# Kernel optimization log

Measured on AMD Instinct MI355X. Metric: run time of the kernel, lower is better.

## Reference

```python
import jax, jax.numpy as jnp
import numpy as np

DIM = 2048
N_HEADS = 16
Q_LORA = 1536
KV_LORA = 512
NOPE = 128
ROPE = 64
QK_D = NOPE + ROPE  # 192
V_D = 128
EPS = 1e-6
B, S = 2, 2048


def rmsnorm(x, w, eps=EPS):
    return x * jax.lax.rsqrt(jnp.mean(x * x, axis=-1, keepdims=True) + eps) * w


def rotate_pe(x, cos, sin):
    # x: [B, S, H, ROPE]; cos/sin: [S, ROPE] -> broadcast [1, S, 1, ROPE]
    c = cos[None, :, None, :]
    s = sin[None, :, None, :]
    x1, x2 = jnp.split(x, 2, axis=-1)
    rot = jnp.concatenate([-x2, x1], axis=-1)
    return x * c + rot * s


def setup_inputs() -> dict:
    key = jax.random.key(0)
    ks = jax.random.split(key, 8)
    std = 0.02
    x = jax.random.normal(ks[0], (B, S, DIM), dtype=jnp.float32)
    # proper rotary tables
    inv_freq = 1.0 / (10000.0 ** (np.arange(0, ROPE, 2, dtype=np.float32) / ROPE))
    t = np.arange(S, dtype=np.float32)
    freqs = np.outer(t, inv_freq)  # [S, ROPE/2]
    emb = np.concatenate([freqs, freqs], axis=-1)  # [S, ROPE]
    cos = jnp.asarray(np.cos(emb))
    sin = jnp.asarray(np.sin(emb))
    wq_a = jax.random.normal(ks[1], (Q_LORA, DIM), dtype=jnp.float32) * std
    q_norm_w = jnp.ones((Q_LORA,), dtype=jnp.float32)
    wq_b = jax.random.normal(ks[2], (N_HEADS * QK_D, Q_LORA), dtype=jnp.float32) * std
    wkv_a = jax.random.normal(ks[3], (KV_LORA + ROPE, DIM), dtype=jnp.float32) * std
    kv_norm_w = jnp.ones((KV_LORA,), dtype=jnp.float32)
    wkv_b = jax.random.normal(ks[4], (N_HEADS * (NOPE + V_D), KV_LORA), dtype=jnp.float32) * std
    wo = jax.random.normal(ks[5], (DIM, N_HEADS * V_D), dtype=jnp.float32) * std
    return {"x": x, "cos": cos, "sin": sin, "wq_a": wq_a, "q_norm_w": q_norm_w,
            "wq_b": wq_b, "wkv_a": wkv_a, "kv_norm_w": kv_norm_w, "wkv_b": wkv_b, "wo": wo}


def mla_forward(x, cos, sin, wq_a, q_norm_w, wq_b, wkv_a, kv_norm_w, wkv_b, wo):
    bsz, seqlen, _ = x.shape
    scale = QK_D ** (-0.5)
    # Q path: low-rank down-proj -> RMSNorm -> up-proj
    q = rmsnorm(x @ wq_a.T, q_norm_w) @ wq_b.T
    q = q.reshape(bsz, seqlen, N_HEADS, QK_D)
    q_nope, q_pe = q[..., :NOPE], q[..., NOPE:]
    q_pe = rotate_pe(q_pe, cos, sin)
    q = jnp.concatenate([q_nope, q_pe], axis=-1)
    # KV path: shared low-rank latent + single rope slice
    kv = x @ wkv_a.T  # [B, S, KV_LORA + ROPE]
    kv_c, k_pe = kv[..., :KV_LORA], kv[..., KV_LORA:]
    k_pe = rotate_pe(k_pe[:, :, None, :], cos, sin)  # [B, S, 1, ROPE]
    kvb = rmsnorm(kv_c, kv_norm_w) @ wkv_b.T
    kvb = kvb.reshape(bsz, seqlen, N_HEADS, NOPE + V_D)
    k_nope, v = kvb[..., :NOPE], kvb[..., NOPE:]
    k = jnp.concatenate([k_nope, jnp.broadcast_to(k_pe, (bsz, seqlen, N_HEADS, ROPE))], axis=-1)
    # causal attention
    scores = jnp.einsum('bqhd,bkhd->bhqk', q, k) * scale
    mask = jnp.tril(jnp.ones((seqlen, seqlen), dtype=bool))
    scores = jnp.where(mask[None, None], scores, jnp.finfo(scores.dtype).min)
    p = jax.nn.softmax(scores, axis=-1)
    out = jnp.einsum('bhqk,bkhd->bqhd', p, v)
    out = out.reshape(bsz, seqlen, N_HEADS * V_D)
    return out @ wo.T


def reference(x, cos, sin, wq_a, q_norm_w, wq_b, wkv_a, kv_norm_w, wkv_b, wo):
    return mla_forward(x, cos, sin, wq_a, q_norm_w, wq_b, wkv_a, kv_norm_w, wkv_b, wo)
```

## Files before the change

kernel.cpp:

```cpp
#include <hip/hip_runtime.h>

typedef unsigned short u16;
typedef __attribute__((ext_vector_type(8))) short short8;
typedef __attribute__((ext_vector_type(4))) float floatx4;

__device__ __forceinline__ float bf2f(u16 u) {
  union { unsigned int i; float f; } v; v.i = ((unsigned int)u) << 16; return v.f;
}
__device__ __forceinline__ u16 f2bf(float f) {
  union { float f; unsigned int i; } v; v.f = f;
  unsigned int u = v.i;
  u += 0x7fffu + ((u >> 16) & 1u);
  return (u16)(u >> 16);
}

__device__ __forceinline__ void gld_lds16(const void* g, void* l) {
  __builtin_amdgcn_global_load_lds(
      (const __attribute__((address_space(1))) unsigned int*)g,
      (__attribute__((address_space(3))) unsigned int*)l, 16, 0, 0);
}

__global__ __launch_bounds__(256) void repack_all_k(
    const float* __restrict__ x, const float* __restrict__ wqa,
    const float* __restrict__ wkva, const float* __restrict__ wqb,
    const float* __restrict__ wkvb, const float* __restrict__ wo,
    u16* __restrict__ xb, u16* __restrict__ wcat, u16* __restrict__ wqbb,
    u16* __restrict__ wkbb, u16* __restrict__ wob) {
  long i = ((long)blockIdx.x * 256 + threadIdx.x) * 4;
  int region = blockIdx.y;
  const float* s = nullptr; u16* d = nullptr; long n = 0;
  switch (region) {
    case 0: s = x;    d = xb;   n = 4096L * 2048; break;
    case 1: s = nullptr; d = wcat; n = 2176L * 2048; break;
    case 2: s = wqb;  d = wqbb; n = 3072L * 1536; break;
    case 3: s = wkvb; d = wkbb; n = 4096L * 512;  break;
    case 4: s = wo;   d = wob;  n = 2048L * 2048; break;
  }
  if (i >= n) return;
  float4 v;
  if (region == 1) {
    long r = i >> 11, c = i & 2047;
    if (r < 1536)      v = *(const float4*)(wqa + r * 2048 + c);
    else if (r < 2112) v = *(const float4*)(wkva + (r - 1536) * 2048 + c);
    else               v = (float4){0.f, 0.f, 0.f, 0.f};
  } else {
    v = *(const float4*)(s + i);
  }
  d[i + 0] = f2bf(v.x); d[i + 1] = f2bf(v.y);
  d[i + 2] = f2bf(v.z); d[i + 3] = f2bf(v.w);
}

template <int OUT_F32>
__device__ __forceinline__ void gemm_tile(
    const u16* __restrict__ A, int lda, const u16* __restrict__ W, int ldw,
    void* __restrict__ Cv, int ldc, int K, int bm, int bn,
    u16* Asm, u16* Bsm) {
  int tid = threadIdx.x;
  int lane = tid & 63, w = tid >> 6;
  int wm = (w >> 1) * 64, wn = (w & 1) * 64;

  floatx4 acc[4][4];
#pragma unroll
  for (int i = 0; i < 4; i++)
#pragma unroll
    for (int j = 0; j < 4; j++) acc[i][j] = (floatx4){0.f, 0.f, 0.f, 0.f};

  int sr = lane >> 2;
  int sc = (lane & 3) * 8;
  int fr = lane & 15;
  int fq = (lane >> 4) * 8;

  for (int k0 = 0; k0 < K; k0 += 32) {
#pragma unroll
    for (int c = 0; c < 2; c++) {
      int row = 32 * w + 16 * c + sr;
      gld_lds16(A + (size_t)(bm + row) * lda + k0 + sc, &Asm[(32 * w + 16 * c) * 32]);
      gld_lds16(W + (size_t)(bn + row) * ldw + k0 + sc, &Bsm[(32 * w + 16 * c) * 32]);
    }
    __syncthreads();
    short8 af[4], bfr[4];
#pragma unroll
    for (int i = 0; i < 4; i++)
      af[i] = *(const short8*)&Asm[(wm + i * 16 + fr) * 32 + fq];
#pragma unroll
    for (int j = 0; j < 4; j++)
      bfr[j] = *(const short8*)&Bsm[(wn + j * 16 + fr) * 32 + fq];
#pragma unroll
    for (int i = 0; i < 4; i++)
#pragma unroll
      for (int j = 0; j < 4; j++)
        acc[i][j] = __builtin_amdgcn_mfma_f32_16x16x32_bf16(af[i], bfr[j], acc[i][j], 0, 0, 0);
    __syncthreads();
  }

  int cr = (lane >> 4) * 4, cc = lane & 15;
#pragma unroll
  for (int i = 0; i < 4; i++)
#pragma unroll
    for (int j = 0; j < 4; j++) {
      int col = bn + wn + j * 16 + cc;
#pragma unroll
      for (int r = 0; r < 4; r++) {
        size_t row = (size_t)(bm + wm + i * 16 + cr + r);
        if (OUT_F32) ((float*)Cv)[row * ldc + col] = acc[i][j][r];
        else         ((u16*)Cv)[row * ldc + col] = f2bf(acc[i][j][r]);
      }
    }
}

template <int OUT_F32>
__global__ __launch_bounds__(256) void gemm_bt_mfma(
    const u16* __restrict__ A, int lda,
    const u16* __restrict__ W, int ldw,
    void* __restrict__ Cv, int ldc, int K) {
  __shared__ u16 Asm[128 * 32];
  __shared__ u16 Bsm[128 * 32];
  gemm_tile<OUT_F32>(A, lda, W, ldw, Cv, ldc, K, blockIdx.y * 128, blockIdx.x * 128, Asm, Bsm);
}

__global__ __launch_bounds__(256) void gemm_dual_mfma(
    const u16* __restrict__ A1, int lda1, const u16* __restrict__ W1, int ldw1,
    u16* __restrict__ C1, int ldc1, int K1, int nt1,
    const u16* __restrict__ A2, int lda2, const u16* __restrict__ W2, int ldw2,
    u16* __restrict__ C2, int ldc2, int K2) {
  __shared__ u16 Asm[128 * 32];
  __shared__ u16 Bsm[128 * 32];
  int bx = blockIdx.x;
  if (bx < nt1)
    gemm_tile<0>(A1, lda1, W1, ldw1, C1, ldc1, K1, blockIdx.y * 128, bx * 128, Asm, Bsm);
  else
    gemm_tile<0>(A2, lda2, W2, ldw2, C2, ldc2, K2, blockIdx.y * 128, (bx - nt1) * 128, Asm, Bsm);
}

__global__ __launch_bounds__(256) void normrope_k(
    u16* __restrict__ qkv, const float* __restrict__ qnw,
    const float* __restrict__ kvnw, const float* __restrict__ cosb,
    const float* __restrict__ sinb, int S) {
  int row = blockIdx.x, tid = threadIdx.x;
  u16* p = qkv + (size_t)row * 2176;
  float s1 = 0.f, s2 = 0.f;
#pragma unroll
  for (int it = 0; it < 6; it++) { float v = bf2f(p[tid + 256 * it]); s1 += v * v; }
#pragma unroll
  for (int it = 0; it < 2; it++) { float v = bf2f(p[1536 + tid + 256 * it]); s2 += v * v; }
  for (int off = 32; off > 0; off >>= 1) {
    s1 += __shfl_down(s1, off);
    s2 += __shfl_down(s2, off);
  }
  __shared__ float red1[4], red2[4];
  if ((tid & 63) == 0) { red1[tid >> 6] = s1; red2[tid >> 6] = s2; }
  __syncthreads();
  float inv1 = rsqrtf((red1[0] + red1[1] + red1[2] + red1[3]) / 1536.f + 1e-6f);
  float inv2 = rsqrtf((red2[0] + red2[1] + red2[2] + red2[3]) / 512.f + 1e-6f);
#pragma unroll
  for (int it = 0; it < 6; it++) {
    int i = tid + 256 * it;
    p[i] = f2bf(bf2f(p[i]) * inv1 * qnw[i]);
  }
#pragma unroll
  for (int it = 0; it < 2; it++) {
    int i = tid + 256 * it;
    p[1536 + i] = f2bf(bf2f(p[1536 + i]) * inv2 * kvnw[i]);
  }
  if (tid < 32) {
    int pos = row % S;
    float c1 = cosb[pos * 64 + tid];
    float c2 = cosb[pos * 64 + tid + 32];
    float sn1 = sinb[pos * 64 + tid];
    float sn2 = sinb[pos * 64 + tid + 32];
    float x1 = bf2f(p[2048 + tid]), x2 = bf2f(p[2048 + tid + 32]);
    p[2048 + tid]      = f2bf(x1 * c1 - x2 * sn1);
    p[2048 + tid + 32] = f2bf(x2 * c2 + x1 * sn2);
  }
}

__global__ __launch_bounds__(256) void rope_k(
    u16* __restrict__ base, int row_stride, int head_stride, int head_off,
    const float* __restrict__ cosb, const float* __restrict__ sinb, int S) {
  int t = blockIdx.x;
  int h = blockIdx.y * 8 + (threadIdx.x >> 5);
  int i = threadIdx.x & 31;
  int pos = t % S;
  u16* p = base + (size_t)t * row_stride + h * head_stride + head_off;
  float c1 = cosb[pos * 64 + i];
  float c2 = cosb[pos * 64 + i + 32];
  float s1 = sinb[pos * 64 + i];
  float s2 = sinb[pos * 64 + i + 32];
  float x1 = bf2f(p[i]), x2 = bf2f(p[i + 32]);
  p[i]      = f2bf(x1 * c1 - x2 * s1);
  p[i + 32] = f2bf(x2 * c2 + x1 * s2);
}

__global__ __launch_bounds__(256) void vtrans_k(
    const u16* __restrict__ kvb, u16* __restrict__ vt, int S) {
  int tb = blockIdx.x, h = blockIdx.y, b = blockIdx.z;
  __shared__ __align__(16) u16 Ts[64][136];
  int tid = threadIdx.x;
#pragma unroll
  for (int it = 0; it < 4; it++) {
    int e = tid + 256 * it;
    int tok = e >> 4, c = e & 15;
    short8 v = *(const short8*)(kvb + (size_t)(b * S + tb * 64 + tok) * 4096 + h * 256 + 128 + c * 8);
    *(short8*)&Ts[tok][c * 8] = v;
  }
  __syncthreads();
  int vd = tid >> 1, half = (tid & 1) * 32;
  u16 tmp[32];
#pragma unroll
  for (int j = 0; j < 32; j++) tmp[j] = Ts[half + j][vd];
  u16* dst = vt + ((size_t)((b * 16 + h) * 128) + vd) * S + tb * 64 + half;
#pragma unroll
  for (int c = 0; c < 4; c++)
    *(short8*)(dst + c * 8) = *(short8*)&tmp[c * 8];
}

#define AT_BK 64
__global__ __launch_bounds__(256) void attn_mfma(
    const u16* __restrict__ qf, const u16* __restrict__ kvb,
    const u16* __restrict__ kpe, int kpe_stride, const u16* __restrict__ vt,
    u16* __restrict__ at, int S) {
  int id = blockIdx.x;
  int pair = id >> 5, hb = id & 31;
  int h = hb & 15, b = hb >> 4;
  int NT = S / AT_BK;
  int tid = threadIdx.x, lane = tid & 63, w = tid >> 6;
  int fr = lane & 15, fq = lane >> 4;
  int fs = fr & 7;

  __shared__ __align__(16) u16 Ksn[AT_BK * 128];
  __shared__ __align__(16) u16 Ksp[AT_BK * 64];
  __shared__ __align__(16) u16 Vts[128 * AT_BK];
  __shared__ __align__(16) u16 Ps[64 * AT_BK];

  const float scale = 0.07216878364870323f;

  for (int p = 0; p < 2; p++) {
    int qt = p ? (NT - 1 - pair) : pair;
    int q0 = qt * 64;

    short8 qfrag[6];
    {
      const u16* qrow = qf + (size_t)(b * S + q0 + w * 16 + fr) * 3072 + h * 192 + fq * 8;
#pragma unroll
      for (int ks = 0; ks < 6; ks++) qfrag[ks] = *(const short8*)(qrow + ks * 32);
    }

    floatx4 acc_o[8];
#pragma unroll
    for (int j = 0; j < 8; j++) acc_o[j] = (floatx4){0.f, 0.f, 0.f, 0.f};
    float m_r[4], l_r[4];
#pragma unroll
    for (int r = 0; r < 4; r++) { m_r[r] = -3e38f; l_r[r] = 0.f; }

    for (int kt = 0; kt <= qt; kt++) {
      int k0 = kt * AT_BK;
      size_t tokbase = (size_t)(b * S + k0);
#pragma unroll
      for (int c = 0; c < 4; c++) {
        int row = w * 16 + c * 4 + (lane >> 4);
        int cg = (lane & 15) ^ (row & 7);
        gld_lds16(kvb + (tokbase + row) * 4096 + h * 256 + cg * 8,
                  &Ksn[(w * 16 + c * 4) * 128]);
      }
#pragma unroll
      for (int c = 0; c < 2; c++) {
        int row = w * 16 + c * 8 + (lane >> 3);
        int cg = (lane & 7) ^ (row & 7);
        gld_lds16(kpe + (tokbase + row) * kpe_stride + cg * 8,
                  &Ksp[(w * 16 + c * 8) * 64]);
      }
#pragma unroll
      for (int c = 0; c < 4; c++) {
        int vd = w * 32 + c * 8 + (lane >> 3);
        int cg = (lane & 7) ^ (vd & 7);
        gld_lds16(vt + ((size_t)((b * 16 + h) * 128) + vd) * S + k0 + cg * 8,
                  &Vts[(w * 32 + c * 8) * 64]);
      }
      __syncthreads();

      floatx4 accs[4];
#pragma unroll
      for (int nt = 0; nt < 4; nt++) accs[nt] = (floatx4){0.f, 0.f, 0.f, 0.f};
      __builtin_amdgcn_s_setprio(1);
#pragma unroll
      for (int nt = 0; nt < 4; nt++) {
#pragma unroll
        for (int ks = 0; ks < 4; ks++) {
          short8 bf = *(const short8*)&Ksn[(nt * 16 + fr) * 128 + ((ks * 4 + fq) ^ fs) * 8];
          accs[nt] = __builtin_amdgcn_mfma_f32_16x16x32_bf16(qfrag[ks], bf, accs[nt], 0, 0, 0);
        }
#pragma unroll
        for (int ks = 0; ks < 2; ks++) {
          short8 bf = *(const short8*)&Ksp[(nt * 16 + fr) * 64 + ((ks * 4 + fq) ^ fs) * 8];
          accs[nt] = __builtin_amdgcn_mfma_f32_16x16x32_bf16(qfrag[4 + ks], bf, accs[nt], 0, 0, 0);
        }
      }
      __builtin_amdgcn_s_setprio(0);

      bool diag = (kt == qt);
#pragma unroll
      for (int nt = 0; nt < 4; nt++)
#pragma unroll
        for (int r = 0; r < 4; r++) {
          float s = accs[nt][r] * scale;
          if (diag) {
            int col = nt * 16 + fr;
            int row = fq * 4 + r;
            if (k0 + col > q0 + w * 16 + row) s = -3e38f;
          }
          accs[nt][r] = s;
        }

      float mx4[4];
      int grow = 0;
#pragma unroll
      for (int r = 0; r < 4; r++) {
        float mx = fmaxf(fmaxf(accs[0][r], accs[1][r]), fmaxf(accs[2][r], accs[3][r]));
        mx = fmaxf(mx, __shfl_xor(mx, 1));
        mx = fmaxf(mx, __shfl_xor(mx, 2));
        mx = fmaxf(mx, __shfl_xor(mx, 4));
        mx = fmaxf(mx, __shfl_xor(mx, 8));
        mx4[r] = mx;
        grow |= (mx > m_r[r] + 8.f) ? 1 : 0;
      }
      bool resc = __any(grow);
      float alpha[4];
      if (resc) {
#pragma unroll
        for (int r = 0; r < 4; r++) {
          float mnew = fmaxf(m_r[r], mx4[r]);
          alpha[r] = __expf(m_r[r] - mnew);
          m_r[r] = mnew;
          l_r[r] *= alpha[r];
        }
      }
#pragma unroll
      for (int nt = 0; nt < 4; nt++)
#pragma unroll
        for (int r = 0; r < 4; r++) {
          float pv = __expf(accs[nt][r] - m_r[r]);
          l_r[r] += pv;
          int row_p = w * 16 + fq * 4 + r;
          int col = nt * 16 + fr;
          Ps[row_p * 64 + (((col >> 3) ^ (row_p & 7)) * 8) + (col & 7)] = f2bf(pv);
        }
      __syncthreads();

      if (resc) {
#pragma unroll
        for (int j = 0; j < 8; j++)
#pragma unroll
          for (int r = 0; r < 4; r++) acc_o[j][r] *= alpha[r];
      }
      short8 pf0 = *(const short8*)&Ps[(w * 16 + fr) * 64 + (fq ^ fs) * 8];
      short8 pf1 = *(const short8*)&Ps[(w * 16 + fr) * 64 + ((4 + fq) ^ fs) * 8];
      __builtin_amdgcn_s_setprio(1);
#pragma unroll
      for (int j = 0; j < 8; j++) {
        short8 v0 = *(const short8*)&Vts[(j * 16 + fr) * 64 + (fq ^ fs) * 8];
        short8 v1 = *(const short8*)&Vts[(j * 16 + fr) * 64 + ((4 + fq) ^ fs) * 8];
        acc_o[j] = __builtin_amdgcn_mfma_f32_16x16x32_bf16(pf0, v0, acc_o[j], 0, 0, 0);
        acc_o[j] = __builtin_amdgcn_mfma_f32_16x16x32_bf16(pf1, v1, acc_o[j], 0, 0, 0);
      }
      __builtin_amdgcn_s_setprio(0);
      __syncthreads();
    }

    float inv_l[4];
#pragma unroll
    for (int r = 0; r < 4; r++) {
      float sm = l_r[r];
      sm += __shfl_xor(sm, 1);
      sm += __shfl_xor(sm, 2);
      sm += __shfl_xor(sm, 4);
      sm += __shfl_xor(sm, 8);
      inv_l[r] = 1.f / sm;
    }
#pragma unroll
    for (int j = 0; j < 8; j++)
#pragma unroll
      for (int r = 0; r < 4; r++) {
        size_t row = (size_t)(b * S + q0 + w * 16 + fq * 4 + r);
        at[row * 2048 + h * 128 + j * 16 + fr] = f2bf(acc_o[j][r] * inv_l[r]);
      }
  }
}

extern "C" void kernel_launch(void* const* d_in, const int* in_sizes, int n_in,
                              void* d_out, int out_size, void* d_ws, size_t ws_size,
                              hipStream_t stream) {
  (void)in_sizes; (void)n_in; (void)out_size; (void)ws_size;
  const float* x     = (const float*)d_in[0];
  const float* cosb  = (const float*)d_in[1];
  const float* sinb  = (const float*)d_in[2];
  const float* wq_a  = (const float*)d_in[3];
  const float* qnw   = (const float*)d_in[4];
  const float* wq_b  = (const float*)d_in[5];
  const float* wkv_a = (const float*)d_in[6];
  const float* kvnw  = (const float*)d_in[7];
  const float* wkv_b = (const float*)d_in[8];
  const float* wo    = (const float*)d_in[9];
  float* out = (float*)d_out;
  const int B = 2, S = 2048, T = B * S;

  char* wsb = (char*)d_ws;
  size_t off = 0;
  u16* xb   = (u16*)(wsb + off); off += (size_t)T * 2048 * 2;
  u16* wcat = (u16*)(wsb + off); off += (size_t)2176 * 2048 * 2;
  u16* wqbb = (u16*)(wsb + off); off += (size_t)3072 * 1536 * 2;
  u16* wkbb = (u16*)(wsb + off); off += (size_t)4096 * 512 * 2;
  u16* wob  = (u16*)(wsb + off); off += (size_t)2048 * 2048 * 2;
  u16* qkv  = (u16*)(wsb + off); off += (size_t)T * 2176 * 2;
  u16* qf   = (u16*)(wsb + off); off += (size_t)T * 3072 * 2;
  u16* kvb  = (u16*)(wsb + off); off += (size_t)T * 4096 * 2;
  u16* at   = (u16*)(wsb + off); off += (size_t)T * 2048 * 2;
  u16* vt   = xb;

  repack_all_k<<<dim3(8192, 5), 256, 0, stream>>>(
      x, wq_a, wkv_a, wq_b, wkv_b, wo, xb, wcat, wqbb, wkbb, wob);

  gemm_bt_mfma<0><<<dim3(2176 / 128, T / 128), 256, 0, stream>>>(xb, 2048, wcat, 2048, qkv, 2176, 2048);
  normrope_k<<<T, 256, 0, stream>>>(qkv, qnw, kvnw, cosb, sinb, S);
  gemm_dual_mfma<<<dim3(3072 / 128 + 4096 / 128, T / 128), 256, 0, stream>>>(
      qkv, 2176, wqbb, 1536, qf, 3072, 1536, 3072 / 128,
      qkv + 1536, 2176, wkbb, 512, kvb, 4096, 512);
  rope_k<<<dim3(T, 2), 256, 0, stream>>>(qf, 3072, 192, 128, cosb, sinb, S);
  vtrans_k<<<dim3(S / 64, 16, B), 256, 0, stream>>>(kvb, vt, S);
  attn_mfma<<<dim3((S / 128) * 32), 256, 0, stream>>>(qf, kvb, qkv + 2048, 2176, vt, at, S);
  gemm_bt_mfma<1><<<dim3(2048 / 128, T / 128), 256, 0, stream>>>(at, 2048, wob, 2048, out, 2048, 2048);
}
```

Measured before the change: 468.3 us.

## Replace GEMMs with 256x256 double-buffered swizzled-LDS pipelined MFMA kernel

All dense projections now use a 256x256 tile kernel with 512 threads, 64-wide K slabs held in double-buffered LDS with an XOR swizzle. Global-to-LDS loads for the next slab are issued between MFMA phases, with explicit waitcnt, barriers and setprio. The q/kv latent buffer is padded from 2176 to 2304 columns so the first GEMM tiles evenly. This aims to raise data reuse per load, avoid LDS bank conflicts, and overlap memory traffic with compute. The cost is more LDS per block (128 KB), fewer blocks in the grid, and some wasted compute on the zero-padded columns.

```diff
diff --git a/kernel.cpp b/kernel.cpp
--- a/kernel.cpp
+++ b/kernel.cpp
@@ -31,7 +31,7 @@
   const float* s = nullptr; u16* d = nullptr; long n = 0;
   switch (region) {
     case 0: s = x;    d = xb;   n = 4096L * 2048; break;
-    case 1: s = nullptr; d = wcat; n = 2176L * 2048; break;
+    case 1: s = nullptr; d = wcat; n = 2304L * 2048; break;
     case 2: s = wqb;  d = wqbb; n = 3072L * 1536; break;
     case 3: s = wkvb; d = wkbb; n = 4096L * 512;  break;
     case 4: s = wo;   d = wob;  n = 2048L * 2048; break;
@@ -50,86 +50,155 @@
   d[i + 2] = f2bf(v.z); d[i + 3] = f2bf(v.w);
 }
 
+#define SBAR()   __builtin_amdgcn_s_barrier()
+#define SCHED0() __builtin_amdgcn_sched_barrier(0)
+
+#define GPHASE(LAc, LBc, QQ, STAGE_STMT, WAIT_STMT)                              \
+  {                                                                              \
+    short8 a00 = *(const short8*)&(LAc)[agbase + (2*(QQ)) * 1024 + g0];          \
+    short8 a01 = *(const short8*)&(LAc)[agbase + (2*(QQ)) * 1024 + g1];          \
+    short8 a10 = *(const short8*)&(LAc)[agbase + (2*(QQ)+1) * 1024 + g0];        \
+    short8 a11 = *(const short8*)&(LAc)[agbase + (2*(QQ)+1) * 1024 + g1];        \
+    if ((QQ) == 0) {                                                             \
+      _Pragma("unroll")                                                          \
+      for (int fj = 0; fj < 4; ++fj) {                                           \
+        bfrg[fj][0] = *(const short8*)&(LBc)[bgbase + fj * 1024 + g0];           \
+        bfrg[fj][1] = *(const short8*)&(LBc)[bgbase + fj * 1024 + g1];           \
+      }                                                                          \
+    }                                                                            \
+    STAGE_STMT;                                                                  \
+    WAIT_STMT;                                                                   \
+    SCHED0();                                                                    \
+    SBAR();                                                                      \
+    asm volatile("s_waitcnt lgkmcnt(0)" ::: "memory");                           \
+    SCHED0();                                                                    \
+    __builtin_amdgcn_s_setprio(1);                                               \
+    _Pragma("unroll")                                                            \
+    for (int fj = 0; fj < 4; ++fj) {                                             \
+      acc[2*(QQ)][fj]   = __builtin_amdgcn_mfma_f32_16x16x32_bf16(a00, bfrg[fj][0], acc[2*(QQ)][fj],   0, 0, 0); \
+      acc[2*(QQ)][fj]   = __builtin_amdgcn_mfma_f32_16x16x32_bf16(a01, bfrg[fj][1], acc[2*(QQ)][fj],   0, 0, 0); \
+      acc[2*(QQ)+1][fj] = __builtin_amdgcn_mfma_f32_16x16x32_bf16(a10, bfrg[fj][0], acc[2*(QQ)+1][fj], 0, 0, 0); \
+      acc[2*(QQ)+1][fj] = __builtin_amdgcn_mfma_f32_16x16x32_bf16(a11, bfrg[fj][1], acc[2*(QQ)+1][fj], 0, 0, 0); \
+    }                                                                            \
+    __builtin_amdgcn_s_setprio(0);                                               \
+    SCHED0();                                                                    \
+    SBAR();                                                                      \
+  }
+
 template <int OUT_F32>
-__device__ __forceinline__ void gemm_tile(
+__device__ __forceinline__ void gemm256_tile(
     const u16* __restrict__ A, int lda, const u16* __restrict__ W, int ldw,
     void* __restrict__ Cv, int ldc, int K, int bm, int bn,
-    u16* Asm, u16* Bsm) {
+    u16* __restrict__ LA, u16* __restrict__ LB) {
   int tid = threadIdx.x;
   int lane = tid & 63, w = tid >> 6;
-  int wm = (w >> 1) * 64, wn = (w & 1) * 64;
-
-  floatx4 acc[4][4];
-#pragma unroll
-  for (int i = 0; i < 4; i++)
+  int wr = w >> 2, wc = w & 3;
+  int fr = lane & 15, fq = lane >> 4;
+
+  int srow = lane >> 3;
+  int sgl  = (lane & 7) ^ srow;
+
+  int agbase = (wr * 128 + fr) * 64;
+  int bgbase = (wc * 64 + fr) * 64;
+  int g0 = ((0 * 4 + fq) ^ (fr & 7)) * 8;
+  int g1 = ((1 * 4 + fq) ^ (fr & 7)) * 8;
+
+  floatx4 acc[8][4];
+#pragma unroll
+  for (int i = 0; i < 8; i++)
 #pragma unroll
     for (int j = 0; j < 4; j++) acc[i][j] = (floatx4){0.f, 0.f, 0.f, 0.f};
 
-  int sr = lane >> 2;
-  int sc = (lane & 3) * 8;
-  int fr = lane & 15;
-  int fq = (lane >> 4) * 8;
-
-  for (int k0 = 0; k0 < K; k0 += 32) {
-#pragma unroll
-    for (int c = 0; c < 2; c++) {
-      int row = 32 * w + 16 * c + sr;
-      gld_lds16(A + (size_t)(bm + row) * lda + k0 + sc, &Asm[(32 * w + 16 * c) * 32]);
-      gld_lds16(W + (size_t)(bn + row) * ldw + k0 + sc, &Bsm[(32 * w + 16 * c) * 32]);
-    }
-    __syncthreads();
-    short8 af[4], bfr[4];
-#pragma unroll
-    for (int i = 0; i < 4; i++)
-      af[i] = *(const short8*)&Asm[(wm + i * 16 + fr) * 32 + fq];
-#pragma unroll
-    for (int j = 0; j < 4; j++)
-      bfr[j] = *(const short8*)&Bsm[(wn + j * 16 + fr) * 32 + fq];
-#pragma unroll
-    for (int i = 0; i < 4; i++)
-#pragma unroll
-      for (int j = 0; j < 4; j++)
-        acc[i][j] = __builtin_amdgcn_mfma_f32_16x16x32_bf16(af[i], bfr[j], acc[i][j], 0, 0, 0);
-    __syncthreads();
+  auto stA = [&](int buf, int kt, int half) {
+#pragma unroll
+    for (int j = 0; j < 2; ++j) {
+      int rbase = half * 128 + (w * 2 + j) * 8;
+      gld_lds16(A + (size_t)(bm + rbase + srow) * lda + kt * 64 + sgl * 8,
+                (void*)&LA[buf * 16384 + rbase * 64]);
+    }
+  };
+  auto stB = [&](int buf, int kt, int half) {
+#pragma unroll
+    for (int j = 0; j < 2; ++j) {
+      int rbase = half * 128 + (w * 2 + j) * 8;
+      gld_lds16(W + (size_t)(bn + rbase + srow) * ldw + kt * 64 + sgl * 8,
+                (void*)&LB[buf * 16384 + rbase * 64]);
+    }
+  };
+
+  const u16* LA0 = LA;           const u16* LB0 = LB;
+  const u16* LA1 = LA + 16384;   const u16* LB1 = LB + 16384;
+
+  stB(0, 0, 0); stB(0, 0, 1);
+  stA(0, 0, 0); stA(0, 0, 1);
+  stB(1, 1, 0); stB(1, 1, 1);
+  asm volatile("s_waitcnt vmcnt(4)" ::: "memory");
+  SCHED0();
+  SBAR();
+
+  int NI = K >> 7;
+  for (int i = 0; i < NI; ++i) {
+    bool notlast = (i + 1 < NI);
+    int t0 = 2 * i;
+    {
+      short8 bfrg[4][2];
+      GPHASE(LA0, LB0, 0, stA(1, t0 + 1, 0), );
+      GPHASE(LA0, LB0, 1, stA(1, t0 + 1, 1), );
+      GPHASE(LA0, LB0, 2, if (notlast) stB(0, t0 + 2, 0), );
+      GPHASE(LA0, LB0, 3, if (notlast) stB(0, t0 + 2, 1),
+             if (notlast) { asm volatile("s_waitcnt vmcnt(4)" ::: "memory"); }
+             else         { asm volatile("s_waitcnt vmcnt(0)" ::: "memory"); });
+    }
+    {
+      short8 bfrg[4][2];
+      GPHASE(LA1, LB1, 0, if (notlast) stA(0, t0 + 2, 0), );
+      GPHASE(LA1, LB1, 1, if (notlast) stA(0, t0 + 2, 1), );
+      GPHASE(LA1, LB1, 2, if (notlast) stB(1, t0 + 3, 0), );
+      GPHASE(LA1, LB1, 3, if (notlast) stB(1, t0 + 3, 1),
+             if (notlast) { asm volatile("s_waitcnt vmcnt(4)" ::: "memory"); });
+    }
   }
 
   int cr = (lane >> 4) * 4, cc = lane & 15;
 #pragma unroll
-  for (int i = 0; i < 4; i++)
-#pragma unroll
-    for (int j = 0; j < 4; j++) {
-      int col = bn + wn + j * 16 + cc;
-#pragma unroll
-      for (int r = 0; r < 4; r++) {
-        size_t row = (size_t)(bm + wm + i * 16 + cr + r);
-        if (OUT_F32) ((float*)Cv)[row * ldc + col] = acc[i][j][r];
-        else         ((u16*)Cv)[row * ldc + col] = f2bf(acc[i][j][r]);
+  for (int fi = 0; fi < 8; ++fi)
+#pragma unroll
+    for (int fj = 0; fj < 4; ++fj) {
+      int col = bn + wc * 64 + fj * 16 + cc;
+#pragma unroll
+      for (int r = 0; r < 4; ++r) {
+        size_t row = (size_t)(bm + wr * 128 + fi * 16 + cr + r);
+        if (OUT_F32) ((float*)Cv)[row * ldc + col] = acc[fi][fj][r];
+        else         ((u16*)Cv)[row * ldc + col] = f2bf(acc[fi][fj][r]);
       }
     }
 }
 
 template <int OUT_F32>
-__global__ __launch_bounds__(256) void gemm_bt_mfma(
+__global__ __launch_bounds__(512, 2) void gemm256_k(
     const u16* __restrict__ A, int lda,
     const u16* __restrict__ W, int ldw,
     void* __restrict__ Cv, int ldc, int K) {
-  __shared__ u16 Asm[128 * 32];
-  __shared__ u16 Bsm[128 * 32];
-  gemm_tile<OUT_F32>(A, lda, W, ldw, Cv, ldc, K, blockIdx.y * 128, blockIdx.x * 128, Asm, Bsm);
-}
-
-__global__ __launch_bounds__(256) void gemm_dual_mfma(
+  __shared__ __align__(16) u16 LAs[2][256 * 64];
+  __shared__ __align__(16) u16 LBs[2][256 * 64];
+  gemm256_tile<OUT_F32>(A, lda, W, ldw, Cv, ldc, K,
+                        blockIdx.y * 256, blockIdx.x * 256, &LAs[0][0], &LBs[0][0]);
+}
+
+__global__ __launch_bounds__(512, 2) void gemm256_dual(
     const u16* __restrict__ A1, int lda1, const u16* __restrict__ W1, int ldw1,
     u16* __restrict__ C1, int ldc1, int K1, int nt1,
     const u16* __restrict__ A2, int lda2, const u16* __restrict__ W2, int ldw2,
     u16* __restrict__ C2, int ldc2, int K2) {
-  __shared__ u16 Asm[128 * 32];
-  __shared__ u16 Bsm[128 * 32];
+  __shared__ __align__(16) u16 LAs[2][256 * 64];
+  __shared__ __align__(16) u16 LBs[2][256 * 64];
   int bx = blockIdx.x;
   if (bx < nt1)
-    gemm_tile<0>(A1, lda1, W1, ldw1, C1, ldc1, K1, blockIdx.y * 128, bx * 128, Asm, Bsm);
+    gemm256_tile<0>(A1, lda1, W1, ldw1, C1, ldc1, K1,
+                    blockIdx.y * 256, bx * 256, &LAs[0][0], &LBs[0][0]);
   else
-    gemm_tile<0>(A2, lda2, W2, ldw2, C2, ldc2, K2, blockIdx.y * 128, (bx - nt1) * 128, Asm, Bsm);
+    gemm256_tile<0>(A2, lda2, W2, ldw2, C2, ldc2, K2,
+                    blockIdx.y * 256, (bx - nt1) * 256, &LAs[0][0], &LBs[0][0]);
 }
 
 __global__ __launch_bounds__(256) void normrope_k(
@@ -137,7 +206,7 @@
     const float* __restrict__ kvnw, const float* __restrict__ cosb,
     const float* __restrict__ sinb, int S) {
   int row = blockIdx.x, tid = threadIdx.x;
-  u16* p = qkv + (size_t)row * 2176;
+  u16* p = qkv + (size_t)row * 2304;
   float s1 = 0.f, s2 = 0.f;
 #pragma unroll
   for (int it = 0; it < 6; it++) { float v = bf2f(p[tid + 256 * it]); s1 += v * v; }
@@ -406,11 +475,11 @@
   char* wsb = (char*)d_ws;
   size_t off = 0;
   u16* xb   = (u16*)(wsb + off); off += (size_t)T * 2048 * 2;
-  u16* wcat = (u16*)(wsb + off); off += (size_t)2176 * 2048 * 2;
+  u16* wcat = (u16*)(wsb + off); off += (size_t)2304 * 2048 * 2;
   u16* wqbb = (u16*)(wsb + off); off += (size_t)3072 * 1536 * 2;
   u16* wkbb = (u16*)(wsb + off); off += (size_t)4096 * 512 * 2;
   u16* wob  = (u16*)(wsb + off); off += (size_t)2048 * 2048 * 2;
-  u16* qkv  = (u16*)(wsb + off); off += (size_t)T * 2176 * 2;
+  u16* qkv  = (u16*)(wsb + off); off += (size_t)T * 2304 * 2;
   u16* qf   = (u16*)(wsb + off); off += (size_t)T * 3072 * 2;
   u16* kvb  = (u16*)(wsb + off); off += (size_t)T * 4096 * 2;
   u16* at   = (u16*)(wsb + off); off += (size_t)T * 2048 * 2;
@@ -419,13 +488,13 @@
   repack_all_k<<<dim3(8192, 5), 256, 0, stream>>>(
       x, wq_a, wkv_a, wq_b, wkv_b, wo, xb, wcat, wqbb, wkbb, wob);
 
-  gemm_bt_mfma<0><<<dim3(2176 / 128, T / 128), 256, 0, stream>>>(xb, 2048, wcat, 2048, qkv, 2176, 2048);
+  gemm256_k<0><<<dim3(2304 / 256, T / 256), 512, 0, stream>>>(xb, 2048, wcat, 2048, qkv, 2304, 2048);
   normrope_k<<<T, 256, 0, stream>>>(qkv, qnw, kvnw, cosb, sinb, S);
-  gemm_dual_mfma<<<dim3(3072 / 128 + 4096 / 128, T / 128), 256, 0, stream>>>(
-      qkv, 2176, wqbb, 1536, qf, 3072, 1536, 3072 / 128,
-      qkv + 1536, 2176, wkbb, 512, kvb, 4096, 512);
+  gemm256_dual<<<dim3(3072 / 256 + 4096 / 256, T / 256), 512, 0, stream>>>(
+      qkv, 2304, wqbb, 1536, qf, 3072, 1536, 3072 / 256,
+      qkv + 1536, 2304, wkbb, 512, kvb, 4096, 512);
   rope_k<<<dim3(T, 2), 256, 0, stream>>>(qf, 3072, 192, 128, cosb, sinb, S);
   vtrans_k<<<dim3(S / 64, 16, B), 256, 0, stream>>>(kvb, vt, S);
-  attn_mfma<<<dim3((S / 128) * 32), 256, 0, stream>>>(qf, kvb, qkv + 2048, 2176, vt, at, S);
-  gemm_bt_mfma<1><<<dim3(2048 / 128, T / 128), 256, 0, stream>>>(at, 2048, wob, 2048, out, 2048, 2048);
-}
+  attn_mfma<<<dim3((S / 128) * 32), 256, 0, stream>>>(qf, kvb, qkv + 2048, 2304, vt, at, S);
+  gemm256_k<1><<<dim3(2048 / 256, T / 256), 512, 0, stream>>>(at, 2048, wob, 2048, out, 2048, 2048);
+}
```

Result: no change. 464.0 us (-0.9%).
